# Performance work log

Measured on AMD Instinct MI355X. Metric: run time of the kernel, lower is better.

Reference implementation:

```python
import jax, jax.numpy as jnp
import numpy as np
import math

H = 4096; NH = 32; QLR = 1536; KVLR = 512
DN = 128; DR = 64; DV = 128; QD = DN + DR  # q_head_dim = 192
B = 1; S = 2048
BASE = 50000.0; FACTOR = 32.0; ORIG_MAX = 4096; BETA_FAST = 32.0; BETA_SLOW = 1.0
EPS = 1e-6
_M = 0.1 * 1.0 * math.log(FACTOR) + 1.0  # yarn mscale (mscale_all_dim=1)
SCALE = (QD ** -0.5) * _M * _M


def _yarn_cos_sin(seq_len):
    dim = DR
    f = np.arange(0, dim, 2, dtype=np.float32) / dim
    freq_extra = 1.0 / BASE ** f
    freq_inter = 1.0 / (FACTOR * BASE ** f)
    def corr(nr):
        return dim * math.log(ORIG_MAX / (nr * 2 * math.pi)) / (2 * math.log(BASE))
    low = max(math.floor(corr(BETA_FAST)), 0)
    high = min(math.ceil(corr(BETA_SLOW)), dim - 1)
    hi = high + 0.001 if low == high else float(high)
    ramp = np.clip((np.arange(dim // 2, dtype=np.float32) - low) / (hi - low), 0.0, 1.0)
    inv_freq_mask = 1.0 - ramp
    inv_freq = freq_inter * (1.0 - inv_freq_mask) + freq_extra * inv_freq_mask
    t = np.arange(seq_len, dtype=np.float32)
    fr = np.outer(t, inv_freq)
    emb = np.concatenate([fr, fr], axis=-1)
    # mscale ratio = get_mscale(f,1)/get_mscale(f,1) = 1.0
    return jnp.asarray(np.cos(emb)), jnp.asarray(np.sin(emb))


def _rms(x, w):
    v = jnp.mean(x.astype(jnp.float32) ** 2, axis=-1, keepdims=True)
    return w * (x.astype(jnp.float32) * jax.lax.rsqrt(v + EPS)).astype(x.dtype)


def _reorder(x):
    # interleaved -> [evens, odds] (matches view(d//2,2).transpose.reshape)
    d = x.shape[-1]
    x = x.reshape(x.shape[:-1] + (d // 2, 2))
    return jnp.concatenate([x[..., 0], x[..., 1]], axis=-1)


def _rotate_half(x):
    h = x.shape[-1] // 2
    return jnp.concatenate([-x[..., h:], x[..., :h]], axis=-1)


def _rope(x, cos, sin):
    x = _reorder(x)
    return x * cos + _rotate_half(x) * sin


def setup_inputs() -> dict:
    key = jax.random.key(0)
    ks = jax.random.split(key, 6)
    hs = jax.random.normal(ks[0], (B, S, H), dtype=jnp.float32)
    causal = jnp.tril(jnp.ones((S, S), dtype=bool))
    mask = jnp.where(causal, 0.0, -1e9).astype(jnp.float32)[None, None]
    pos = jnp.broadcast_to(jnp.arange(S, dtype=jnp.int64 if jax.config.jax_enable_x64 else jnp.int32), (B, S))
    def w(k, shape, fan_in):
        return jax.random.normal(k, shape, dtype=jnp.float32) * (fan_in ** -0.5)
    return {
        "hidden_states": hs,
        "attention_mask": mask,
        "position_ids": pos,
        "q_a_w": w(ks[1], (QLR, H), H),
        "q_a_ln_w": jnp.ones((QLR,), jnp.float32),
        "q_b_w": w(ks[2], (NH * QD, QLR), QLR),
        "kv_a_w": w(ks[3], (KVLR + DR, H), H),
        "kv_a_ln_w": jnp.ones((KVLR,), jnp.float32),
        "kv_b_w": w(ks[4], (NH * (DN + DV), KVLR), KVLR),
        "o_w": w(ks[5], (H, NH * DV), NH * DV),
    }


def reference(hidden_states, attention_mask, position_ids, q_a_w, q_a_ln_w, q_b_w, kv_a_w, kv_a_ln_w, kv_b_w, o_w):
    b, s, _ = hidden_states.shape
    q = _rms(hidden_states @ q_a_w.T, q_a_ln_w) @ q_b_w.T
    q = q.reshape(b, s, NH, QD).transpose(0, 2, 1, 3)          # [b,h,s,192]
    q_nope, q_pe = q[..., :DN], q[..., DN:]
    ckv = hidden_states @ kv_a_w.T                              # [b,s,576]
    comp, k_pe = ckv[..., :KVLR], ckv[..., KVLR:]
    k_pe = k_pe.reshape(b, s, 1, DR).transpose(0, 2, 1, 3)      # [b,1,s,64]
    kv = (_rms(comp, kv_a_ln_w) @ kv_b_w.T).reshape(b, s, NH, DN + DV).transpose(0, 2, 1, 3)
    k_nope, v = kv[..., :DN], kv[..., DN:]
    cos, sin = _yarn_cos_sin(s)
    cos = cos[position_ids][:, None]                            # [b,1,s,64]
    sin = sin[position_ids][:, None]
    q_pe = _rope(q_pe, cos, sin)
    k_pe = _rope(k_pe, cos, sin)
    qs = jnp.concatenate([q_nope, q_pe], axis=-1)               # [b,h,s,192]
    ks = jnp.concatenate([k_nope, jnp.broadcast_to(k_pe, (b, NH, s, DR))], axis=-1)
    aw = jnp.einsum('bhqd,bhkd->bhqk', qs, ks) * SCALE
    aw = jax.nn.softmax((aw + attention_mask).astype(jnp.float32), axis=-1).astype(hidden_states.dtype)
    out = jnp.einsum('bhqk,bhkd->bhqd', aw, v)                  # [b,h,s,128]
    out = out.transpose(0, 2, 1, 3).reshape(b, s, NH * DV)
    return out @ o_w.T
```

## Files before the change

kernel.cpp:

```cpp
#include <hip/hip_runtime.h>
#include <hip/hip_fp16.h>

typedef _Float16 f16x8 __attribute__((ext_vector_type(8)));
typedef float f32x4 __attribute__((ext_vector_type(4)));

#define DEV __device__ __forceinline__

typedef const __attribute__((address_space(1))) void gvoid_t;
typedef __attribute__((address_space(3))) void lvoid_t;

DEV void gload16(const void* g, void* l) {
  __builtin_amdgcn_global_load_lds((gvoid_t*)g, (lvoid_t*)l, 16, 0, 0);
}

DEV f32x4 mfma16(f16x8 a, f16x8 b, f32x4 c) {
  return __builtin_amdgcn_mfma_f32_16x16x32_f16(a, b, c, 0, 0, 0);
}

__global__ __launch_bounds__(256) void cvt_kernel(const float* __restrict__ s,
                                                  __half* __restrict__ d, int n4) {
  int stride = gridDim.x * 256;
  for (int i = blockIdx.x * 256 + threadIdx.x; i < n4; i += stride) {
    float4 v = ((const float4*)s)[i];
    __align__(8) __half a[4] = {__float2half(v.x), __float2half(v.y),
                                __float2half(v.z), __float2half(v.w)};
    *((uint2*)(d + (size_t)i * 4)) = *((uint2*)a);
  }
}

__global__ __launch_bounds__(256) void cvt5_kernel(const float* __restrict__ s0,
                                                   const float* __restrict__ s1,
                                                   const float* __restrict__ s2,
                                                   const float* __restrict__ s3,
                                                   const float* __restrict__ s4,
                                                   __half* __restrict__ d0, __half* __restrict__ d1,
                                                   __half* __restrict__ d2, __half* __restrict__ d3,
                                                   __half* __restrict__ d4) {
  const int c0 = 2097152, c1 = 3670016, c2 = 4259840, c3 = 6619136, c4 = 7667712;
  int stride = gridDim.x * 256;
  for (int i = blockIdx.x * 256 + threadIdx.x; i < c4; i += stride) {
    const float* s;
    __half* d;
    int j;
    if (i < c0) { s = s0; d = d0; j = i; }
    else if (i < c1) { s = s1; d = d1; j = i - c0; }
    else if (i < c2) { s = s2; d = d2; j = i - c1; }
    else if (i < c3) { s = s3; d = d3; j = i - c2; }
    else { s = s4; d = d4; j = i - c3; }
    float4 v = ((const float4*)s)[j];
    __align__(8) __half a[4] = {__float2half(v.x), __float2half(v.y),
                                __float2half(v.z), __float2half(v.w)};
    *((uint2*)(d + (size_t)j * 4)) = *((uint2*)a);
  }
}

template <int W>
__global__ __launch_bounds__(256) void rms_kernel(const float* __restrict__ x, int ldx,
                                                  const float* __restrict__ wgt,
                                                  __half* __restrict__ y, int ldy) {
  const int row = blockIdx.x, tid = threadIdx.x;
  const float4* xr = (const float4*)(x + (size_t)row * ldx);
  float4 v0 = make_float4(0.f, 0.f, 0.f, 0.f), v1 = v0;
  if (tid < W / 4) v0 = xr[tid];
  if (tid + 256 < W / 4) v1 = xr[tid + 256];
  float ss = v0.x * v0.x + v0.y * v0.y + v0.z * v0.z + v0.w * v0.w +
             v1.x * v1.x + v1.y * v1.y + v1.z * v1.z + v1.w * v1.w;
  for (int mm = 1; mm <= 32; mm <<= 1) ss += __shfl_xor(ss, mm);
  __shared__ float sred[4];
  if ((tid & 63) == 0) sred[tid >> 6] = ss;
  __syncthreads();
  float rs = 1.0f / sqrtf((sred[0] + sred[1] + sred[2] + sred[3]) * (1.0f / (float)W) + 1e-6f);
  __half* yr = y + (size_t)row * ldy;
  if (tid < W / 4) {
    int j = tid * 4;
    yr[j + 0] = __float2half(wgt[j + 0] * v0.x * rs);
    yr[j + 1] = __float2half(wgt[j + 1] * v0.y * rs);
    yr[j + 2] = __float2half(wgt[j + 2] * v0.z * rs);
    yr[j + 3] = __float2half(wgt[j + 3] * v0.w * rs);
  }
  if (tid + 256 < W / 4) {
    int j = (tid + 256) * 4;
    yr[j + 0] = __float2half(wgt[j + 0] * v1.x * rs);
    yr[j + 1] = __float2half(wgt[j + 1] * v1.y * rs);
    yr[j + 2] = __float2half(wgt[j + 2] * v1.z * rs);
    yr[j + 3] = __float2half(wgt[j + 3] * v1.w * rs);
  }
}

__global__ __launch_bounds__(256) void rope_table_kernel(const int* __restrict__ pos,
                                                         float2* __restrict__ cs) {
  int i = blockIdx.x * 256 + threadIdx.x;
  int row = i >> 5, j = i & 31;
  double f = (double)j * (1.0 / 32.0);
  double fe = exp(-f * 10.81977828441028);
  double fi = fe * (1.0 / 32.0);
  double ramp = fmin(fmax(((double)j - 8.0) * (1.0 / 12.0), 0.0), 1.0);
  double inv = fi * ramp + fe * (1.0 - ramp);
  double ang = (double)pos[row] * inv;
  cs[i] = make_float2((float)cos(ang), (float)sin(ang));
}

__global__ __launch_bounds__(256) void rope_q_kernel(const __half* __restrict__ qpe,
                                                     const float2* __restrict__ cs,
                                                     __half* __restrict__ Qb, float qscale) {
  int i = blockIdx.x * 256 + threadIdx.x;
  int row = i >> 10, rem = i & 1023, h = rem >> 5, j = rem & 31;
  float x0 = __half2float(qpe[(size_t)row * 2048 + h * 64 + 2 * j]);
  float x1 = __half2float(qpe[(size_t)row * 2048 + h * 64 + 2 * j + 1]);
  float2 c = cs[row * 32 + j];
  float o0 = (x0 * c.x - x1 * c.y) * qscale;
  float o1 = (x1 * c.x + x0 * c.y) * qscale;
  __half* dst = Qb + ((size_t)h * 2048 + row) * 192;
  dst[128 + j] = __float2half(o0);
  dst[160 + j] = __float2half(o1);
}

__global__ __launch_bounds__(256) void rope_k_kernel(const float* __restrict__ kpe, int ld,
                                                     const float2* __restrict__ cs,
                                                     __half* __restrict__ Kb) {
  int i = blockIdx.x * 256 + threadIdx.x;
  int row = i >> 10, rem = i & 1023, h = rem >> 5, j = rem & 31;
  float x0 = kpe[(size_t)row * ld + 2 * j];
  float x1 = kpe[(size_t)row * ld + 2 * j + 1];
  float2 c = cs[row * 32 + j];
  __half* dst = Kb + ((size_t)h * 2048 + row) * 192;
  dst[128 + j] = __float2half(x0 * c.x - x1 * c.y);
  dst[160 + j] = __float2half(x1 * c.x + x0 * c.y);
}

template <int EPI>
__global__ __launch_bounds__(256) void gemm128(const __half* __restrict__ A, int lda,
                                               const __half* __restrict__ B, int K, int Ncols,
                                               float* __restrict__ Cf, int ldc,
                                               __half* __restrict__ O1, __half* __restrict__ O2,
                                               float qscale) {
  __shared__ __align__(16) char As[32768];
  __shared__ __align__(16) char Bs[32768];
  const int tid = threadIdx.x;
  const int lane = tid & 63, w = tid >> 6;
  const int l15 = lane & 15, g = lane >> 4;
  const int wr = w >> 1, wc = w & 1;
  const int nwg = gridDim.x * gridDim.y;
  int wg = blockIdx.y * gridDim.x + blockIdx.x;
  wg = (wg & 7) * (nwg >> 3) + (wg >> 3);
  const int m0 = (wg / gridDim.x) * 128, n0 = (wg % gridDim.x) * 128;
  const int srow = lane >> 3;
  const int scol = ((lane & 7) ^ srow) * 8;
  f32x4 acc[4][4] = {};
  const int nt = K >> 6;

  auto stage = [&](int t, int buf) {
    const __half* Ab = A + t * 64 + scol;
    const __half* Bb = B + t * 64 + scol;
#pragma unroll
    for (int cc = 0; cc < 4; ++cc) {
      int ch = w * 4 + cc;
      gload16(Ab + (size_t)(m0 + ch * 8 + srow) * lda, As + buf * 16384 + ch * 1024);
      gload16(Bb + (size_t)(n0 + ch * 8 + srow) * K, Bs + buf * 16384 + ch * 1024);
    }
  };

  stage(0, 0);
  __syncthreads();

  for (int t = 0; t < nt; ++t) {
    const int buf = t & 1;
    if (t + 1 < nt) stage(t + 1, buf ^ 1);
    const char* Ab = As + buf * 16384;
    const char* Bb = Bs + buf * 16384;
#pragma unroll
    for (int kk = 0; kk < 2; ++kk) {
      f16x8 af[4], bf[4];
#pragma unroll
      for (int m = 0; m < 4; ++m) {
        int r = wr * 64 + m * 16 + l15;
        af[m] = *(const f16x8*)(Ab + r * 128 + (((kk << 2) | g) ^ (r & 7)) * 16);
      }
#pragma unroll
      for (int n = 0; n < 4; ++n) {
        int r = wc * 64 + n * 16 + l15;
        bf[n] = *(const f16x8*)(Bb + r * 128 + (((kk << 2) | g) ^ (r & 7)) * 16);
      }
#pragma unroll
      for (int m = 0; m < 4; ++m)
#pragma unroll
        for (int n = 0; n < 4; ++n) acc[m][n] = mfma16(af[m], bf[n], acc[m][n]);
    }
    __syncthreads();
  }

#pragma unroll
  for (int m = 0; m < 4; ++m)
#pragma unroll
    for (int n = 0; n < 4; ++n)
#pragma unroll
      for (int i = 0; i < 4; ++i) {
        int row = m0 + wr * 64 + m * 16 + g * 4 + i;
        int col = n0 + wc * 64 + n * 16 + l15;
        float v = acc[m][n][i];
        if (EPI == 0) {
          if (col < Ncols) Cf[(size_t)row * ldc + col] = v;
        } else if (EPI == 2) {
          int h = col / 192, d = col - h * 192;
          if (d < 128)
            O1[((size_t)h * 2048 + row) * 192 + d] = __float2half(v * qscale);
          else
            O2[(size_t)row * 2048 + h * 64 + (d - 128)] = __float2half(v);
        } else if (EPI == 3) {
          int h = col >> 8, d = col & 255;
          if (d < 128)
            O1[((size_t)h * 2048 + row) * 192 + d] = __float2half(v);
          else
            O2[((size_t)h * 128 + (d - 128)) * 2048 + row] = __float2half(v);
        }
      }
}

__global__ __launch_bounds__(256) void attn_kernel(const __half* __restrict__ Q,
                                                   const __half* __restrict__ K,
                                                   const __half* __restrict__ Vt,
                                                   __half* __restrict__ Out) {
  __shared__ __align__(16) char Klds[2 * 64 * 384];
  __shared__ __align__(16) char Vlds[128 * 128];
  __shared__ __align__(16) __half Plds[4][16][72];
  int wg = blockIdx.y * gridDim.x + blockIdx.x;
  wg = (wg & 7) * 64 + (wg >> 3);
  const int pr = wg & 15, h = wg >> 4;
  const int tid = threadIdx.x, lane = tid & 63, w = tid >> 6;
  const int l15 = lane & 15, g = lane >> 4;

  const char* Kg = (const char*)(K + (size_t)h * 2048 * 192);
  const char* Vg = (const char*)(Vt + (size_t)h * 128 * 2048);

  int kL[6], kRow[6], kSS[6];
#pragma unroll
  for (int cc = 0; cc < 6; ++cc) {
    int c = w * 6 + cc;
    int L = c * 64 + lane;
    int row = (L * 2731) >> 16;
    int slot = L - row * 24;
    kL[cc] = c;
    kRow[cc] = row;
    kSS[cc] = (slot & ~7) | ((slot ^ row) & 7);
  }

  for (int ht = 0; ht < 2; ++ht) {
    const int qt = ht ? (31 - pr) : pr;
    const int q0 = qt * 64;
    const int nt = qt + 1;

    const __half* Qh = Q + ((size_t)h * 2048 + q0 + w * 16 + l15) * 192;
    f16x8 qf[6];
#pragma unroll
    for (int kc = 0; kc < 6; ++kc) qf[kc] = *(const f16x8*)(Qh + kc * 32 + g * 8);

    f32x4 acc[8] = {};
    float m_i[4], l_i[4];
#pragma unroll
    for (int i = 0; i < 4; ++i) { m_i[i] = -1e30f; l_i[i] = 0.f; }

#pragma unroll
    for (int cc = 0; cc < 6; ++cc)
      gload16(Kg + (size_t)kRow[cc] * 384 + kSS[cc] * 16, Klds + kL[cc] * 1024);
    __syncthreads();

    for (int t = 0; t < nt; ++t) {
      const int kv0 = t * 64;
      const char* Kcur = Klds + (t & 1) * 24576;

#pragma unroll
      for (int cc = 0; cc < 4; ++cc) {
        int c = w * 4 + cc;
        int L = c * 64 + lane;
        int d = L >> 3, slot = L & 7;
        int ss = slot ^ (d & 7);
        gload16(Vg + ((size_t)d * 2048 + kv0) * 2 + ss * 16, Vlds + c * 1024);
      }
      if (t + 1 < nt) {
        char* Knxt = Klds + ((t + 1) & 1) * 24576;
#pragma unroll
        for (int cc = 0; cc < 6; ++cc)
          gload16(Kg + (size_t)(kv0 + 64 + kRow[cc]) * 384 + kSS[cc] * 16,
                  Knxt + kL[cc] * 1024);
      }

      f32x4 s[4] = {};
      __builtin_amdgcn_s_setprio(1);
#pragma unroll
      for (int kc = 0; kc < 6; ++kc) {
#pragma unroll
        for (int n = 0; n < 4; ++n) {
          int krow = n * 16 + l15;
          int slot = kc * 4 + g;
          int ss = (slot & ~7) | ((slot ^ krow) & 7);
          f16x8 kf = *(const f16x8*)(Kcur + krow * 384 + ss * 16);
          s[n] = mfma16(qf[kc], kf, s[n]);
        }
      }
      __builtin_amdgcn_s_setprio(0);

      const bool diag = (t == nt - 1);
      float ps[4][4];
      float mt[4] = {-1e30f, -1e30f, -1e30f, -1e30f};
#pragma unroll
      for (int n = 0; n < 4; ++n)
#pragma unroll
        for (int i = 0; i < 4; ++i) {
          float v = s[n][i];
          if (diag) {
            int key = n * 16 + l15, qq = w * 16 + g * 4 + i;
            if (key > qq) v = -1e30f;
          }
          ps[n][i] = v;
          mt[i] = fmaxf(mt[i], v);
        }
#pragma unroll
      for (int mm = 1; mm <= 8; mm <<= 1)
#pragma unroll
        for (int i = 0; i < 4; ++i) mt[i] = fmaxf(mt[i], __shfl_xor(mt[i], mm));
      float corr[4], rsum[4];
#pragma unroll
      for (int i = 0; i < 4; ++i) {
        float mn = fmaxf(m_i[i], mt[i]);
        corr[i] = __expf(m_i[i] - mn);
        m_i[i] = mn;
        rsum[i] = 0.f;
      }
#pragma unroll
      for (int n = 0; n < 4; ++n)
#pragma unroll
        for (int i = 0; i < 4; ++i) {
          float p = __expf(ps[n][i] - m_i[i]);
          ps[n][i] = p;
          rsum[i] += p;
        }
#pragma unroll
      for (int mm = 1; mm <= 8; mm <<= 1)
#pragma unroll
        for (int i = 0; i < 4; ++i) rsum[i] += __shfl_xor(rsum[i], mm);
#pragma unroll
      for (int i = 0; i < 4; ++i) l_i[i] = l_i[i] * corr[i] + rsum[i];
#pragma unroll
      for (int db = 0; db < 8; ++db)
#pragma unroll
        for (int i = 0; i < 4; ++i) acc[db][i] *= corr[i];
#pragma unroll
      for (int n = 0; n < 4; ++n)
#pragma unroll
        for (int i = 0; i < 4; ++i) Plds[w][g * 4 + i][n * 16 + l15] = __float2half(ps[n][i]);

      __syncthreads();

      __builtin_amdgcn_s_setprio(1);
#pragma unroll
      for (int ks = 0; ks < 2; ++ks) {
        f16x8 pa = *(const f16x8*)((const char*)&Plds[w][0][0] + l15 * 144 + ks * 64 + g * 16);
#pragma unroll
        for (int db = 0; db < 8; ++db) {
          int d = db * 16 + l15;
          int ss = (ks * 4 + g) ^ (d & 7);
          f16x8 vf = *(const f16x8*)(Vlds + d * 128 + ss * 16);
          acc[db] = mfma16(pa, vf, acc[db]);
        }
      }
      __builtin_amdgcn_s_setprio(0);
      __syncthreads();
    }

#pragma unroll
    for (int db = 0; db < 8; ++db)
#pragma unroll
      for (int i = 0; i < 4; ++i) {
        int row = q0 + w * 16 + g * 4 + i;
        Out[(size_t)row * 4096 + h * 128 + db * 16 + l15] = __float2half(acc[db][i] / l_i[i]);
      }
  }
}

extern "C" void kernel_launch(void* const* d_in, const int* in_sizes, int n_in,
                              void* d_out, int out_size, void* d_ws, size_t ws_size,
                              hipStream_t stream) {
  (void)in_sizes; (void)n_in; (void)out_size; (void)ws_size;
  const float* hs = (const float*)d_in[0];
  const int* pos = (const int*)d_in[2];
  const float* q_a_w = (const float*)d_in[3];
  const float* q_a_ln = (const float*)d_in[4];
  const float* q_b_w = (const float*)d_in[5];
  const float* kv_a_w = (const float*)d_in[6];
  const float* kv_a_ln = (const float*)d_in[7];
  const float* kv_b_w = (const float*)d_in[8];
  const float* o_w = (const float*)d_in[9];

  char* p = (char*)d_ws;
  auto alloc = [&](size_t sz) { char* r = p; p += (sz + 255) & ~(size_t)255; return r; };
  __half* hs_h = (__half*)alloc((size_t)2048 * 4096 * 2);
  __half* w_qab = (__half*)alloc((size_t)2176 * 4096 * 2);
  __half* w_qb = (__half*)alloc((size_t)6144 * 1536 * 2);
  __half* w_kvb = (__half*)alloc((size_t)8192 * 512 * 2);
  float* qab_f = (float*)alloc((size_t)2048 * 2112 * 4);
  __half* qa_r = (__half*)alloc((size_t)2048 * 1536 * 2);
  __half* kv_r = (__half*)alloc((size_t)2048 * 512 * 2);
  float2* cs_tab = (float2*)alloc((size_t)2048 * 32 * 8);
  __half* Qb = (__half*)alloc((size_t)32 * 2048 * 192 * 2);
  __half* Kb = (__half*)alloc((size_t)32 * 2048 * 192 * 2);
  __half* Vtb = (__half*)alloc((size_t)32 * 128 * 2048 * 2);
  __half* qpe = (__half*)alloc((size_t)2048 * 2048 * 2);
  __half* attn_h = hs_h;
  __half* w_o = Qb;

  constexpr float QSCALE = 0.13086090981960297f;

  cvt5_kernel<<<2048, 256, 0, stream>>>(hs, q_a_w, kv_a_w, q_b_w, kv_b_w,
                                        hs_h, w_qab, w_qab + (size_t)1536 * 4096,
                                        w_qb, w_kvb);
  rope_table_kernel<<<(2048 * 32) / 256, 256, 0, stream>>>(pos, cs_tab);

  gemm128<0><<<dim3(17, 16), 256, 0, stream>>>(hs_h, 4096, w_qab, 4096, 2112, qab_f, 2112,
                                               nullptr, nullptr, 1.f);
  rms_kernel<1536><<<2048, 256, 0, stream>>>(qab_f, 2112, q_a_ln, qa_r, 1536);
  rms_kernel<512><<<2048, 256, 0, stream>>>(qab_f + 1536, 2112, kv_a_ln, kv_r, 512);
  rope_k_kernel<<<(2048 * 1024) / 256, 256, 0, stream>>>(qab_f + 2048, 2112, cs_tab, Kb);
  gemm128<2><<<dim3(48, 16), 256, 0, stream>>>(qa_r, 1536, w_qb, 1536, 6144, nullptr, 0,
                                               Qb, qpe, QSCALE);
  rope_q_kernel<<<(2048 * 1024) / 256, 256, 0, stream>>>(qpe, cs_tab, Qb, QSCALE);
  gemm128<3><<<dim3(64, 16), 256, 0, stream>>>(kv_r, 512, w_kvb, 512, 8192, nullptr, 0,
                                               Kb, Vtb, 1.f);
  attn_kernel<<<dim3(16, 32), 256, 0, stream>>>(Qb, Kb, Vtb, attn_h);
  cvt_kernel<<<2048, 256, 0, stream>>>(o_w, w_o, (int)((size_t)4096 * 4096 / 4));
  gemm128<0><<<dim3(32, 16), 256, 0, stream>>>(attn_h, 4096, w_o, 4096, 4096, (float*)d_out,
                                               4096, nullptr, nullptr, 1.f);
}
```

Baseline: 441.0 us.

## Fuse RMS norms with K rope, widen first GEMM tile, streamline attention softmax

Merges the two RMSNorm kernels and the K-side rope into one per-row kernel, removing two launches and a re-read of the projection output. The GEMM gains a BN template so the first projection uses 192-wide N tiles (11 column blocks instead of 17), cutting the padded wasted work. Attention now works in base-2 exponentials with log2e folded into the Q scale and skips rescaling when the running max grows by 8 or less. The row sum is taken by an extra MFMA against a ones column stored in LDS, and the setprio hints are removed. The lazy rescale trades a little precision headroom for fewer rescale multiplies, and the extra ones column adds a ninth MFMA per PV step.

```diff
diff --git a/kernel.cpp b/kernel.cpp
--- a/kernel.cpp
+++ b/kernel.cpp
@@ -54,36 +54,67 @@
   }
 }
 
-template <int W>
-__global__ __launch_bounds__(256) void rms_kernel(const float* __restrict__ x, int ldx,
-                                                  const float* __restrict__ wgt,
-                                                  __half* __restrict__ y, int ldy) {
+__global__ __launch_bounds__(256) void norm_rope_kernel(const float* __restrict__ qab,
+                                                        const float* __restrict__ q_ln,
+                                                        const float* __restrict__ kv_ln,
+                                                        const float2* __restrict__ cs,
+                                                        __half* __restrict__ qa_r,
+                                                        __half* __restrict__ kv_r,
+                                                        __half* __restrict__ Kb) {
   const int row = blockIdx.x, tid = threadIdx.x;
-  const float4* xr = (const float4*)(x + (size_t)row * ldx);
-  float4 v0 = make_float4(0.f, 0.f, 0.f, 0.f), v1 = v0;
-  if (tid < W / 4) v0 = xr[tid];
-  if (tid + 256 < W / 4) v1 = xr[tid + 256];
-  float ss = v0.x * v0.x + v0.y * v0.y + v0.z * v0.z + v0.w * v0.w +
-             v1.x * v1.x + v1.y * v1.y + v1.z * v1.z + v1.w * v1.w;
-  for (int mm = 1; mm <= 32; mm <<= 1) ss += __shfl_xor(ss, mm);
-  __shared__ float sred[4];
-  if ((tid & 63) == 0) sred[tid >> 6] = ss;
+  const float* xr = qab + (size_t)row * 2112;
+  float4 a0 = ((const float4*)xr)[tid];
+  float4 a1 = make_float4(0.f, 0.f, 0.f, 0.f);
+  float4 b0 = make_float4(0.f, 0.f, 0.f, 0.f);
+  if (tid < 128) {
+    a1 = ((const float4*)xr)[256 + tid];
+    b0 = ((const float4*)(xr + 1536))[tid];
+  }
+  float sq = a0.x * a0.x + a0.y * a0.y + a0.z * a0.z + a0.w * a0.w +
+             a1.x * a1.x + a1.y * a1.y + a1.z * a1.z + a1.w * a1.w;
+  float sk = b0.x * b0.x + b0.y * b0.y + b0.z * b0.z + b0.w * b0.w;
+  for (int mm = 1; mm <= 32; mm <<= 1) {
+    sq += __shfl_xor(sq, mm);
+    sk += __shfl_xor(sk, mm);
+  }
+  __shared__ float r1[4], r2[4];
+  __shared__ __half ro[64];
+  if ((tid & 63) == 0) { r1[tid >> 6] = sq; r2[tid >> 6] = sk; }
+  if (tid < 32) {
+    float x0 = xr[2048 + 2 * tid], x1 = xr[2048 + 2 * tid + 1];
+    float2 c = cs[row * 32 + tid];
+    ro[tid] = __float2half(x0 * c.x - x1 * c.y);
+    ro[32 + tid] = __float2half(x1 * c.x + x0 * c.y);
+  }
   __syncthreads();
-  float rs = 1.0f / sqrtf((sred[0] + sred[1] + sred[2] + sred[3]) * (1.0f / (float)W) + 1e-6f);
-  __half* yr = y + (size_t)row * ldy;
-  if (tid < W / 4) {
+  float rsq = rsqrtf((r1[0] + r1[1] + r1[2] + r1[3]) * (1.f / 1536.f) + 1e-6f);
+  float rsk = rsqrtf((r2[0] + r2[1] + r2[2] + r2[3]) * (1.f / 512.f) + 1e-6f);
+  __half* yq = qa_r + (size_t)row * 1536;
+  {
     int j = tid * 4;
-    yr[j + 0] = __float2half(wgt[j + 0] * v0.x * rs);
-    yr[j + 1] = __float2half(wgt[j + 1] * v0.y * rs);
-    yr[j + 2] = __float2half(wgt[j + 2] * v0.z * rs);
-    yr[j + 3] = __float2half(wgt[j + 3] * v0.w * rs);
-  }
-  if (tid + 256 < W / 4) {
-    int j = (tid + 256) * 4;
-    yr[j + 0] = __float2half(wgt[j + 0] * v1.x * rs);
-    yr[j + 1] = __float2half(wgt[j + 1] * v1.y * rs);
-    yr[j + 2] = __float2half(wgt[j + 2] * v1.z * rs);
-    yr[j + 3] = __float2half(wgt[j + 3] * v1.w * rs);
+    yq[j + 0] = __float2half(q_ln[j + 0] * a0.x * rsq);
+    yq[j + 1] = __float2half(q_ln[j + 1] * a0.y * rsq);
+    yq[j + 2] = __float2half(q_ln[j + 2] * a0.z * rsq);
+    yq[j + 3] = __float2half(q_ln[j + 3] * a0.w * rsq);
+  }
+  if (tid < 128) {
+    int j = 1024 + tid * 4;
+    yq[j + 0] = __float2half(q_ln[j + 0] * a1.x * rsq);
+    yq[j + 1] = __float2half(q_ln[j + 1] * a1.y * rsq);
+    yq[j + 2] = __float2half(q_ln[j + 2] * a1.z * rsq);
+    yq[j + 3] = __float2half(q_ln[j + 3] * a1.w * rsq);
+    __half* yk = kv_r + (size_t)row * 512;
+    int jk = tid * 4;
+    yk[jk + 0] = __float2half(kv_ln[jk + 0] * b0.x * rsk);
+    yk[jk + 1] = __float2half(kv_ln[jk + 1] * b0.y * rsk);
+    yk[jk + 2] = __float2half(kv_ln[jk + 2] * b0.z * rsk);
+    yk[jk + 3] = __float2half(kv_ln[jk + 3] * b0.w * rsk);
+  }
+#pragma unroll
+  for (int it = 0; it < 8; ++it) {
+    int i = it * 256 + tid;
+    int hh = i >> 6, d = i & 63;
+    Kb[((size_t)hh * 2048 + row) * 192 + 128 + d] = ro[d];
   }
 }
 
@@ -115,27 +146,15 @@
   dst[160 + j] = __float2half(o1);
 }
 
-__global__ __launch_bounds__(256) void rope_k_kernel(const float* __restrict__ kpe, int ld,
-                                                     const float2* __restrict__ cs,
-                                                     __half* __restrict__ Kb) {
-  int i = blockIdx.x * 256 + threadIdx.x;
-  int row = i >> 10, rem = i & 1023, h = rem >> 5, j = rem & 31;
-  float x0 = kpe[(size_t)row * ld + 2 * j];
-  float x1 = kpe[(size_t)row * ld + 2 * j + 1];
-  float2 c = cs[row * 32 + j];
-  __half* dst = Kb + ((size_t)h * 2048 + row) * 192;
-  dst[128 + j] = __float2half(x0 * c.x - x1 * c.y);
-  dst[160 + j] = __float2half(x1 * c.x + x0 * c.y);
-}
-
-template <int EPI>
+template <int BN, int EPI>
 __global__ __launch_bounds__(256) void gemm128(const __half* __restrict__ A, int lda,
                                                const __half* __restrict__ B, int K, int Ncols,
                                                float* __restrict__ Cf, int ldc,
                                                __half* __restrict__ O1, __half* __restrict__ O2,
                                                float qscale) {
-  __shared__ __align__(16) char As[32768];
-  __shared__ __align__(16) char Bs[32768];
+  constexpr int NFR = BN / 32;
+  __shared__ __align__(16) char As[2 * 128 * 128];
+  __shared__ __align__(16) char Bs[2 * BN * 128];
   const int tid = threadIdx.x;
   const int lane = tid & 63, w = tid >> 6;
   const int l15 = lane & 15, g = lane >> 4;
@@ -143,10 +162,10 @@
   const int nwg = gridDim.x * gridDim.y;
   int wg = blockIdx.y * gridDim.x + blockIdx.x;
   wg = (wg & 7) * (nwg >> 3) + (wg >> 3);
-  const int m0 = (wg / gridDim.x) * 128, n0 = (wg % gridDim.x) * 128;
+  const int m0 = (wg / gridDim.x) * 128, n0 = (wg % gridDim.x) * BN;
   const int srow = lane >> 3;
   const int scol = ((lane & 7) ^ srow) * 8;
-  f32x4 acc[4][4] = {};
+  f32x4 acc[4][NFR] = {};
   const int nt = K >> 6;
 
   auto stage = [&](int t, int buf) {
@@ -156,7 +175,11 @@
     for (int cc = 0; cc < 4; ++cc) {
       int ch = w * 4 + cc;
       gload16(Ab + (size_t)(m0 + ch * 8 + srow) * lda, As + buf * 16384 + ch * 1024);
-      gload16(Bb + (size_t)(n0 + ch * 8 + srow) * K, Bs + buf * 16384 + ch * 1024);
+    }
+#pragma unroll
+    for (int cc = 0; cc < NFR; ++cc) {
+      int ch = w * NFR + cc;
+      gload16(Bb + (size_t)(n0 + ch * 8 + srow) * K, Bs + buf * (BN * 128) + ch * 1024);
     }
   };
 
@@ -167,24 +190,24 @@
     const int buf = t & 1;
     if (t + 1 < nt) stage(t + 1, buf ^ 1);
     const char* Ab = As + buf * 16384;
-    const char* Bb = Bs + buf * 16384;
+    const char* Bb = Bs + buf * (BN * 128);
 #pragma unroll
     for (int kk = 0; kk < 2; ++kk) {
-      f16x8 af[4], bf[4];
+      f16x8 af[4], bf[NFR];
 #pragma unroll
       for (int m = 0; m < 4; ++m) {
         int r = wr * 64 + m * 16 + l15;
         af[m] = *(const f16x8*)(Ab + r * 128 + (((kk << 2) | g) ^ (r & 7)) * 16);
       }
 #pragma unroll
-      for (int n = 0; n < 4; ++n) {
-        int r = wc * 64 + n * 16 + l15;
+      for (int n = 0; n < NFR; ++n) {
+        int r = wc * (BN / 2) + n * 16 + l15;
         bf[n] = *(const f16x8*)(Bb + r * 128 + (((kk << 2) | g) ^ (r & 7)) * 16);
       }
 #pragma unroll
       for (int m = 0; m < 4; ++m)
 #pragma unroll
-        for (int n = 0; n < 4; ++n) acc[m][n] = mfma16(af[m], bf[n], acc[m][n]);
+        for (int n = 0; n < NFR; ++n) acc[m][n] = mfma16(af[m], bf[n], acc[m][n]);
     }
     __syncthreads();
   }
@@ -192,11 +215,11 @@
 #pragma unroll
   for (int m = 0; m < 4; ++m)
 #pragma unroll
-    for (int n = 0; n < 4; ++n)
+    for (int n = 0; n < NFR; ++n)
 #pragma unroll
       for (int i = 0; i < 4; ++i) {
         int row = m0 + wr * 64 + m * 16 + g * 4 + i;
-        int col = n0 + wc * 64 + n * 16 + l15;
+        int col = n0 + wc * (BN / 2) + n * 16 + l15;
         float v = acc[m][n][i];
         if (EPI == 0) {
           if (col < Ncols) Cf[(size_t)row * ldc + col] = v;
@@ -221,7 +244,7 @@
                                                    const __half* __restrict__ Vt,
                                                    __half* __restrict__ Out) {
   __shared__ __align__(16) char Klds[2 * 64 * 384];
-  __shared__ __align__(16) char Vlds[128 * 128];
+  __shared__ __align__(16) char Vlds[144 * 128];
   __shared__ __align__(16) __half Plds[4][16][72];
   int wg = blockIdx.y * gridDim.x + blockIdx.x;
   wg = (wg & 7) * 64 + (wg >> 3);
@@ -231,6 +254,11 @@
 
   const char* Kg = (const char*)(K + (size_t)h * 2048 * 192);
   const char* Vg = (const char*)(Vt + (size_t)h * 128 * 2048);
+
+  if (tid < 128) {
+    ((uint4*)(Vlds + 16384))[tid] =
+        make_uint4(0x3C003C00u, 0x3C003C00u, 0x3C003C00u, 0x3C003C00u);
+  }
 
   int kL[6], kRow[6], kSS[6];
 #pragma unroll
@@ -254,10 +282,10 @@
 #pragma unroll
     for (int kc = 0; kc < 6; ++kc) qf[kc] = *(const f16x8*)(Qh + kc * 32 + g * 8);
 
-    f32x4 acc[8] = {};
-    float m_i[4], l_i[4];
-#pragma unroll
-    for (int i = 0; i < 4; ++i) { m_i[i] = -1e30f; l_i[i] = 0.f; }
+    f32x4 acc[9] = {};
+    float m_i[4];
+#pragma unroll
+    for (int i = 0; i < 4; ++i) m_i[i] = -1e30f;
 
 #pragma unroll
     for (int cc = 0; cc < 6; ++cc)
@@ -285,7 +313,6 @@
       }
 
       f32x4 s[4] = {};
-      __builtin_amdgcn_s_setprio(1);
 #pragma unroll
       for (int kc = 0; kc < 6; ++kc) {
 #pragma unroll
@@ -297,7 +324,6 @@
           s[n] = mfma16(qf[kc], kf, s[n]);
         }
       }
-      __builtin_amdgcn_s_setprio(0);
 
       const bool diag = (t == nt - 1);
       float ps[4][4];
@@ -318,62 +344,54 @@
       for (int mm = 1; mm <= 8; mm <<= 1)
 #pragma unroll
         for (int i = 0; i < 4; ++i) mt[i] = fmaxf(mt[i], __shfl_xor(mt[i], mm));
-      float corr[4], rsum[4];
+
+      bool ok = true;
+      float nm[4];
 #pragma unroll
       for (int i = 0; i < 4; ++i) {
-        float mn = fmaxf(m_i[i], mt[i]);
-        corr[i] = __expf(m_i[i] - mn);
-        m_i[i] = mn;
-        rsum[i] = 0.f;
+        nm[i] = fmaxf(m_i[i], mt[i]);
+        ok = ok && (mt[i] - m_i[i] <= 8.0f);
+      }
+      if (!__all(ok)) {
+#pragma unroll
+        for (int i = 0; i < 4; ++i) {
+          float c = exp2f(m_i[i] - nm[i]);
+          m_i[i] = nm[i];
+#pragma unroll
+          for (int db = 0; db < 9; ++db) acc[db][i] *= c;
+        }
       }
 #pragma unroll
       for (int n = 0; n < 4; ++n)
 #pragma unroll
-        for (int i = 0; i < 4; ++i) {
-          float p = __expf(ps[n][i] - m_i[i]);
-          ps[n][i] = p;
-          rsum[i] += p;
-        }
-#pragma unroll
-      for (int mm = 1; mm <= 8; mm <<= 1)
-#pragma unroll
-        for (int i = 0; i < 4; ++i) rsum[i] += __shfl_xor(rsum[i], mm);
-#pragma unroll
-      for (int i = 0; i < 4; ++i) l_i[i] = l_i[i] * corr[i] + rsum[i];
-#pragma unroll
-      for (int db = 0; db < 8; ++db)
-#pragma unroll
-        for (int i = 0; i < 4; ++i) acc[db][i] *= corr[i];
-#pragma unroll
-      for (int n = 0; n < 4; ++n)
-#pragma unroll
-        for (int i = 0; i < 4; ++i) Plds[w][g * 4 + i][n * 16 + l15] = __float2half(ps[n][i]);
+        for (int i = 0; i < 4; ++i)
+          Plds[w][g * 4 + i][n * 16 + l15] = __float2half(exp2f(ps[n][i] - m_i[i]));
 
       __syncthreads();
 
-      __builtin_amdgcn_s_setprio(1);
 #pragma unroll
       for (int ks = 0; ks < 2; ++ks) {
         f16x8 pa = *(const f16x8*)((const char*)&Plds[w][0][0] + l15 * 144 + ks * 64 + g * 16);
 #pragma unroll
-        for (int db = 0; db < 8; ++db) {
+        for (int db = 0; db < 9; ++db) {
           int d = db * 16 + l15;
           int ss = (ks * 4 + g) ^ (d & 7);
           f16x8 vf = *(const f16x8*)(Vlds + d * 128 + ss * 16);
           acc[db] = mfma16(pa, vf, acc[db]);
         }
       }
-      __builtin_amdgcn_s_setprio(0);
       __syncthreads();
     }
 
 #pragma unroll
-    for (int db = 0; db < 8; ++db)
-#pragma unroll
-      for (int i = 0; i < 4; ++i) {
+    for (int i = 0; i < 4; ++i) {
+      float inv = 1.0f / acc[8][i];
+#pragma unroll
+      for (int db = 0; db < 8; ++db) {
         int row = q0 + w * 16 + g * 4 + i;
-        Out[(size_t)row * 4096 + h * 128 + db * 16 + l15] = __float2half(acc[db][i] / l_i[i]);
-      }
+        Out[(size_t)row * 4096 + h * 128 + db * 16 + l15] = __float2half(acc[db][i] * inv);
+      }
+    }
   }
 }
 
@@ -408,25 +426,25 @@
   __half* attn_h = hs_h;
   __half* w_o = Qb;
 
-  constexpr float QSCALE = 0.13086090981960297f;
+  constexpr float QSCALE = 0.13086090981960297f * 1.4426950408889634f;
 
   cvt5_kernel<<<2048, 256, 0, stream>>>(hs, q_a_w, kv_a_w, q_b_w, kv_b_w,
                                         hs_h, w_qab, w_qab + (size_t)1536 * 4096,
                                         w_qb, w_kvb);
   rope_table_kernel<<<(2048 * 32) / 256, 256, 0, stream>>>(pos, cs_tab);
 
-  gemm128<0><<<dim3(17, 16), 256, 0, stream>>>(hs_h, 4096, w_qab, 4096, 2112, qab_f, 2112,
-                                               nullptr, nullptr, 1.f);
-  rms_kernel<1536><<<2048, 256, 0, stream>>>(qab_f, 2112, q_a_ln, qa_r, 1536);
-  rms_kernel<512><<<2048, 256, 0, stream>>>(qab_f + 1536, 2112, kv_a_ln, kv_r, 512);
-  rope_k_kernel<<<(2048 * 1024) / 256, 256, 0, stream>>>(qab_f + 2048, 2112, cs_tab, Kb);
-  gemm128<2><<<dim3(48, 16), 256, 0, stream>>>(qa_r, 1536, w_qb, 1536, 6144, nullptr, 0,
-                                               Qb, qpe, QSCALE);
+  gemm128<192, 0><<<dim3(11, 16), 256, 0, stream>>>(hs_h, 4096, w_qab, 4096, 2112, qab_f,
+                                                    2112, nullptr, nullptr, 1.f);
+  norm_rope_kernel<<<2048, 256, 0, stream>>>(qab_f, q_a_ln, kv_a_ln, cs_tab,
+                                             qa_r, kv_r, Kb);
+  gemm128<128, 2><<<dim3(48, 16), 256, 0, stream>>>(qa_r, 1536, w_qb, 1536, 6144, nullptr,
+                                                    0, Qb, qpe, QSCALE);
   rope_q_kernel<<<(2048 * 1024) / 256, 256, 0, stream>>>(qpe, cs_tab, Qb, QSCALE);
-  gemm128<3><<<dim3(64, 16), 256, 0, stream>>>(kv_r, 512, w_kvb, 512, 8192, nullptr, 0,
-                                               Kb, Vtb, 1.f);
+  gemm128<128, 3><<<dim3(64, 16), 256, 0, stream>>>(kv_r, 512, w_kvb, 512, 8192, nullptr,
+                                                    0, Kb, Vtb, 1.f);
   attn_kernel<<<dim3(16, 32), 256, 0, stream>>>(Qb, Kb, Vtb, attn_h);
   cvt_kernel<<<2048, 256, 0, stream>>>(o_w, w_o, (int)((size_t)4096 * 4096 / 4));
-  gemm128<0><<<dim3(32, 16), 256, 0, stream>>>(attn_h, 4096, w_o, 4096, 4096, (float*)d_out,
-                                               4096, nullptr, nullptr, 1.f);
-}
+  gemm128<128, 0><<<dim3(32, 16), 256, 0, stream>>>(attn_h, 4096, w_o, 4096, 4096,
+                                                    (float*)d_out, 4096, nullptr, nullptr,
+                                                    1.f);
+}
```

Measured after the change: 421.1 us. 4.5% less time.
